# Kernel tuning notes

Hardware: AMD Instinct MI355X
Metric: run time of the kernel (lower is better)

## Reference

```python
import jax, jax.numpy as jnp
import numpy as np

N_NODES = 50000
N_EDGES = 400000
NUM_FEATURES = 128
NUM_CLASSES = 40
DIMS = [NUM_FEATURES, 1024, 512, 128]


def _glorot(key, shape):
    fan_in, fan_out = shape
    lim = jnp.sqrt(6.0 / (fan_in + fan_out))
    return jax.random.uniform(key, shape, jnp.float32, -lim, lim)


def setup_inputs() -> dict:
    key = jax.random.key(0)
    ks = jax.random.split(key, 12)
    x = jax.random.normal(ks[0], (N_NODES, NUM_FEATURES), jnp.float32)
    edge_index = jax.random.randint(ks[1], (2, N_EDGES), 0, N_NODES, jnp.int64)
    W1 = _glorot(ks[2], (DIMS[0], DIMS[1])); b1 = jnp.zeros((DIMS[1],), jnp.float32)
    W2 = _glorot(ks[3], (DIMS[1], DIMS[2])); b2 = jnp.zeros((DIMS[2],), jnp.float32)
    W3 = _glorot(ks[4], (DIMS[2], DIMS[3])); b3 = jnp.zeros((DIMS[3],), jnp.float32)
    Wfc = _glorot(ks[5], (DIMS[3], NUM_CLASSES))
    bfc = jnp.zeros((NUM_CLASSES,), jnp.float32)
    return {"x": x, "edge_index": edge_index, "W1": W1, "b1": b1,
            "W2": W2, "b2": b2, "W3": W3, "b3": b3, "Wfc": Wfc, "bfc": bfc}


def _gcn_conv(x, W, b, src, dst, norm, inv_deg, n_nodes):
    # GCNConv: transform, then symmetric-normalized aggregation with self-loops.
    h = x @ W                                   # [N, out]
    msg = h[src] * norm[:, None]                # [E, out] gathered + scaled
    agg = jax.ops.segment_sum(msg, dst, num_segments=n_nodes)
    agg = agg + h * inv_deg[:, None]            # self-loop term: d^-1 * h_i
    return agg + b


def reference(x, edge_index, W1, b1, W2, b2, W3, b3, Wfc, bfc):
    n = x.shape[0]
    src, dst = edge_index[0], edge_index[1]
    # degree including the self-loop (weight 1 per edge + 1 self-loop)
    deg = jax.ops.segment_sum(jnp.ones_like(dst, dtype=x.dtype), dst, num_segments=n) + 1.0
    inv_sqrt = jax.lax.rsqrt(deg)
    norm = inv_sqrt[src] * inv_sqrt[dst]        # [E]
    inv_deg = 1.0 / deg                         # self-loop norm d^-.5 * d^-.5

    h = jax.nn.relu(_gcn_conv(x, W1, b1, src, dst, norm, inv_deg, n))
    h = jax.nn.relu(_gcn_conv(h, W2, b2, src, dst, norm, inv_deg, n))
    h = jax.nn.relu(_gcn_conv(h, W3, b3, src, dst, norm, inv_deg, n))
    return h @ Wfc + bfc
```

## Files before the change

### kernel.cpp

```cpp
#include <hip/hip_runtime.h>
#include <hip/hip_bf16.h>
#include <cstdint>
#include <cstddef>

#define NN 50000
#define NE 400000
typedef long long i64;
typedef unsigned short u16;
typedef __attribute__((ext_vector_type(8))) short bf16x8;
typedef __attribute__((ext_vector_type(8))) unsigned short u16x8;
typedef __attribute__((ext_vector_type(4))) float f32x4;

__device__ inline u16 f2bf(float f) {
    unsigned u = __float_as_uint(f);
    u += 0x7fffu + ((u >> 16) & 1u);
    return (u16)(u >> 16);
}
__device__ inline float bf2f(u16 b) { return __uint_as_float(((unsigned)b) << 16); }

__global__ void k_init(int* __restrict__ deg, int* __restrict__ flag) {
    int i = blockIdx.x * blockDim.x + threadIdx.x;
    if (i < NN) deg[i] = 0;
    if (i == 0) *flag = 0;
}

__global__ void k_detect(const void* __restrict__ ei, int* __restrict__ flag) {
    int i = blockIdx.x * blockDim.x + threadIdx.x;
    if (i < NE) {
        i64 v = ((const i64*)ei)[i];
        if (v < 0 || v >= NN) atomicOr(flag, 1);
    }
}

__device__ inline int edge_at(const void* ei, int f32idx, int half, int i) {
    if (f32idx) return ((const int*)ei)[half * NE + i];
    return (int)((const i64*)ei)[half * NE + i];
}

__global__ void k_hist(const void* __restrict__ ei, const int* __restrict__ flag,
                       int* __restrict__ deg) {
    int i = blockIdx.x * blockDim.x + threadIdx.x;
    if (i < NE) {
        int d = edge_at(ei, *flag, 1, i);
        if ((unsigned)d < NN) atomicAdd(&deg[d], 1);
    }
}

__global__ void k_node_setup(const int* __restrict__ deg, float* __restrict__ inv_sqrt,
                             float* __restrict__ inv_deg) {
    int i = blockIdx.x * blockDim.x + threadIdx.x;
    if (i < NN) {
        float d = (float)deg[i] + 1.0f;
        inv_sqrt[i] = rsqrtf(d);
        inv_deg[i]  = 1.0f / d;
    }
}

#define SB 256
#define NBLK ((NN + SB - 1) / SB)

__global__ __launch_bounds__(SB) void k_scan1(const int* __restrict__ deg,
                                              int* __restrict__ excl,
                                              int* __restrict__ bsum) {
    __shared__ int s[SB];
    int t = threadIdx.x;
    int i = blockIdx.x * SB + t;
    int v = (i < NN) ? deg[i] : 0;
    s[t] = v;
    __syncthreads();
    for (int off = 1; off < SB; off <<= 1) {
        int x = (t >= off) ? s[t - off] : 0;
        __syncthreads();
        s[t] += x;
        __syncthreads();
    }
    if (i < NN) excl[i] = s[t] - v;
    if (t == SB - 1) bsum[blockIdx.x] = s[t];
}

__global__ __launch_bounds__(SB) void k_scan2(int* __restrict__ bsum) {
    __shared__ int s[SB];
    int t = threadIdx.x;
    int v = (t < NBLK) ? bsum[t] : 0;
    s[t] = v;
    __syncthreads();
    for (int off = 1; off < SB; off <<= 1) {
        int x = (t >= off) ? s[t - off] : 0;
        __syncthreads();
        s[t] += x;
        __syncthreads();
    }
    if (t < NBLK) bsum[t] = s[t] - v;
    if (t == NBLK - 1) bsum[NBLK] = s[t];
}

__global__ __launch_bounds__(SB) void k_scan3(int* __restrict__ row_off,
                                              int* __restrict__ cursor,
                                              const int* __restrict__ bsum) {
    int i = blockIdx.x * SB + threadIdx.x;
    if (i < NN) {
        int r = row_off[i] + bsum[blockIdx.x];
        row_off[i] = r;
        cursor[i]  = r;
    }
    if (i == 0) row_off[NN] = bsum[NBLK];
}

__global__ void k_scatter(const void* __restrict__ ei, const int* __restrict__ flag,
                          const float* __restrict__ inv_sqrt,
                          int* __restrict__ cursor, int* __restrict__ ssrc,
                          float* __restrict__ snorm) {
    int i = blockIdx.x * blockDim.x + threadIdx.x;
    if (i < NE) {
        int f = *flag;
        int s = edge_at(ei, f, 0, i);
        int d = edge_at(ei, f, 1, i);
        if ((unsigned)s < NN && (unsigned)d < NN) {
            int pos = atomicAdd(&cursor[d], 1);
            if ((unsigned)pos < NE) {
                ssrc[pos]  = s;
                snorm[pos] = inv_sqrt[s] * inv_sqrt[d];
            }
        }
    }
}

__global__ void k_wt(const float* __restrict__ W, u16* __restrict__ Wt, int K, int N) {
    int i = blockIdx.x * 256 + threadIdx.x;
    if (i < K * N) {
        int k = i / N, n = i - k * N;
        Wt[(size_t)n * K + k] = f2bf(W[i]);
    }
}

template <int W, int TIN, int TOUT, bool BIAS, bool RELU>
__global__ __launch_bounds__(64) void k_agg(const void* __restrict__ Xv, void* __restrict__ Yv,
                      const int* __restrict__ row_off, const int* __restrict__ ssrc,
                      const float* __restrict__ snorm, const float* __restrict__ inv_deg,
                      const float* __restrict__ bias) {
    constexpr int E = W / 64;
    int node = blockIdx.x;
    int lane = threadIdx.x;
    int col = lane * E;
    int beg = row_off[node], end = row_off[node + 1];
    float acc[E];
#pragma unroll
    for (int v = 0; v < E; v++) acc[v] = 0.f;

    auto accum = [&](int srow, float w) {
        if constexpr (TIN == 0) {
            const float* r = (const float*)Xv + (size_t)srow * W + col;
            if constexpr (E == 2) {
                float2 t = *(const float2*)r;
                acc[0] = fmaf(t.x, w, acc[0]);
                acc[1] = fmaf(t.y, w, acc[1]);
            } else {
                float4 t0 = *(const float4*)r;
                float4 t1 = *(const float4*)(r + 4);
                acc[0] = fmaf(t0.x, w, acc[0]); acc[1] = fmaf(t0.y, w, acc[1]);
                acc[2] = fmaf(t0.z, w, acc[2]); acc[3] = fmaf(t0.w, w, acc[3]);
                acc[4] = fmaf(t1.x, w, acc[4]); acc[5] = fmaf(t1.y, w, acc[5]);
                acc[6] = fmaf(t1.z, w, acc[6]); acc[7] = fmaf(t1.w, w, acc[7]);
            }
        } else {
            const u16* r = (const u16*)Xv + (size_t)srow * W + col;
            if constexpr (E == 2) {
                unsigned t = *(const unsigned*)r;
                acc[0] = fmaf(bf2f((u16)(t & 0xffff)), w, acc[0]);
                acc[1] = fmaf(bf2f((u16)(t >> 16)), w, acc[1]);
            } else {
                u16x8 t = *(const u16x8*)r;
#pragma unroll
                for (int j = 0; j < 8; j++) acc[j] = fmaf(bf2f(t[j]), w, acc[j]);
            }
        }
    };

    for (int e = beg; e < end; e++) {
        int s = ssrc[e];
        if ((unsigned)s >= NN) continue;
        accum(s, snorm[e]);
    }
    accum(node, inv_deg[node]);

#pragma unroll
    for (int v = 0; v < E; v++) {
        float val = acc[v];
        if (BIAS) val += bias[col + v];
        if (RELU) val = fmaxf(val, 0.f);
        if constexpr (TOUT == 0) ((float*)Yv)[(size_t)node * W + col + v] = val;
        else ((u16*)Yv)[(size_t)node * W + col + v] = f2bf(val);
    }
}

#define LDS_AS(p) ((__attribute__((address_space(3))) void*)(p))
#define GLB_AS(p) ((const __attribute__((address_space(1))) void*)(p))
#define EPAD 68

template <bool BIAS, bool RELU>
__global__ __launch_bounds__(512, 2) void gemm8(
    const u16* __restrict__ A, const u16* __restrict__ Bt,
    const float* __restrict__ bias, u16* __restrict__ C,
    int M, int N, int K, int nbx) {
    __shared__ __align__(16) char smem[131072];
    char* buf0 = smem;
    char* buf1 = smem + 65536;
    const int tid = threadIdx.x;
    const int lane = tid & 63;
    const int wave = tid >> 6;
    const int wm = wave >> 2;
    const int wn = wave & 3;

    const int nwg = gridDim.x;
    int lg;
    { int q = nwg >> 3, r = nwg & 7, xc = blockIdx.x & 7, pos = blockIdx.x >> 3;
      lg = (xc < r ? xc * (q + 1) : r * (q + 1) + (xc - r) * q) + pos; }
    const int bm = (lg / nbx) * 256;
    const int bn = (lg % nbx) * 256;

    f32x4 acc[8][4];
#pragma unroll
    for (int m = 0; m < 8; m++)
#pragma unroll
        for (int n = 0; n < 4; n++) acc[m][n] = (f32x4)0.f;

    const int rb = tid >> 3;
    const int csw = ((tid & 7) ^ (rb & 7)) << 4;
    const int dstA = rb * 128 + (tid & 7) * 16;
    const size_t sK = (size_t)K * 2;
    const char* Ab = (const char*)A;
    const char* Bb = (const char*)Bt;
    size_t ga[2][2], gb[2][2];
#pragma unroll
    for (int h = 0; h < 2; h++)
#pragma unroll
        for (int j = 0; j < 2; j++) {
            int ar = bm + h * 128 + j * 64 + rb; if (ar >= M) ar = M - 1;
            int br = bn + h * 128 + j * 64 + rb;
            ga[h][j] = (size_t)ar * sK + csw;
            gb[h][j] = (size_t)br * sK + csw;
        }

    auto stA = [&](char* buf, size_t kb, int h) {
        __builtin_amdgcn_global_load_lds(GLB_AS(Ab + ga[h][0] + kb), LDS_AS(buf + h * 16384 + dstA), 16, 0, 0);
        __builtin_amdgcn_global_load_lds(GLB_AS(Ab + ga[h][1] + kb), LDS_AS(buf + h * 16384 + 8192 + dstA), 16, 0, 0);
    };
    auto stB = [&](char* buf, size_t kb, int h) {
        __builtin_amdgcn_global_load_lds(GLB_AS(Bb + gb[h][0] + kb), LDS_AS(buf + 32768 + h * 16384 + dstA), 16, 0, 0);
        __builtin_amdgcn_global_load_lds(GLB_AS(Bb + gb[h][1] + kb), LDS_AS(buf + 32768 + h * 16384 + 8192 + dstA), 16, 0, 0);
    };

    const int fr = lane & 15, g = lane >> 4;
    const int ksw0 = (((0 << 2) + g) ^ (fr & 7)) << 4;
    const int ksw1 = (((1 << 2) + g) ^ (fr & 7)) << 4;
    const int aRow = (wm * 128 + fr) * 128;
    const int bRow = 32768 + (wn * 64 + fr) * 128;

    bf16x8 af[4][2], bf[4][2];
    auto LDA = [&](const char* buf, int mg) {
#pragma unroll
        for (int m = 0; m < 4; m++) {
            af[m][0] = *(const bf16x8*)(buf + aRow + mg * 8192 + m * 2048 + ksw0);
            af[m][1] = *(const bf16x8*)(buf + aRow + mg * 8192 + m * 2048 + ksw1);
        }
    };
    auto LDB = [&](const char* buf, int ng) {
#pragma unroll
        for (int n = 0; n < 2; n++) {
            bf[ng * 2 + n][0] = *(const bf16x8*)(buf + bRow + (ng * 2 + n) * 2048 + ksw0);
            bf[ng * 2 + n][1] = *(const bf16x8*)(buf + bRow + (ng * 2 + n) * 2048 + ksw1);
        }
    };
    auto QMM = [&](int mg, int ng) {
        __builtin_amdgcn_s_setprio(1);
#pragma unroll
        for (int ks = 0; ks < 2; ks++)
#pragma unroll
            for (int m = 0; m < 4; m++)
#pragma unroll
                for (int n = 0; n < 2; n++)
                    acc[mg * 4 + m][ng * 2 + n] = __builtin_amdgcn_mfma_f32_16x16x32_bf16(
                        af[m][ks], bf[ng * 2 + n][ks], acc[mg * 4 + m][ng * 2 + n], 0, 0, 0);
        __builtin_amdgcn_s_setprio(0);
    };

#define BAR  __builtin_amdgcn_s_barrier()
#define LGKM do { asm volatile("s_waitcnt lgkmcnt(0)" ::: "memory"); __builtin_amdgcn_sched_barrier(0); } while (0)

    const int nit = K >> 7;

    stB(buf0, 0, 0); stB(buf0, 0, 1);
    stA(buf0, 0, 0); stA(buf0, 0, 1);
    stB(buf1, 128, 0); stB(buf1, 128, 1);
    asm volatile("s_waitcnt vmcnt(4)" ::: "memory");
    BAR;

    for (int it2 = 0; it2 < nit; ++it2) {
        const bool lastit = (it2 == nit - 1);
        const size_t kb = (size_t)it2 * 256;
        LDA(buf0, 0); LDB(buf0, 0);
        stA(buf1, kb + 128, 0);
        BAR; LGKM; QMM(0, 0); BAR;
        LDB(buf0, 1);
        stA(buf1, kb + 128, 1);
        BAR; LGKM; QMM(0, 1); BAR;
        LDA(buf0, 1);
        if (!lastit) stB(buf0, kb + 256, 0);
        BAR; LGKM; QMM(1, 0); BAR;
        if (!lastit) stB(buf0, kb + 256, 1);
        BAR; QMM(1, 1);
        if (lastit) asm volatile("s_waitcnt vmcnt(0)" ::: "memory");
        else        asm volatile("s_waitcnt vmcnt(4)" ::: "memory");
        BAR;
        LDA(buf1, 0); LDB(buf1, 0);
        if (!lastit) stA(buf0, kb + 256, 0);
        BAR; LGKM; QMM(0, 0); BAR;
        LDB(buf1, 1);
        if (!lastit) stA(buf0, kb + 256, 1);
        BAR; LGKM; QMM(0, 1); BAR;
        LDA(buf1, 1);
        if (!lastit) stB(buf1, kb + 384, 0);
        BAR; LGKM; QMM(1, 0); BAR;
        if (!lastit) stB(buf1, kb + 384, 1);
        BAR; QMM(1, 1);
        if (!lastit) asm volatile("s_waitcnt vmcnt(4)" ::: "memory");
        BAR;
    }

    u16* Es = (u16*)(smem + (size_t)wave * (64 * EPAD * 2));
    const int cr = (lane >> 4) << 2;
    const int cc = lane & 15;
    const int rl = lane >> 3;
    const int c8 = (lane & 7) * 8;
#pragma unroll
    for (int pass = 0; pass < 2; pass++) {
#pragma unroll
        for (int n = 0; n < 4; n++) {
            float bv = BIAS ? bias[bn + wn * 64 + n * 16 + cc] : 0.f;
#pragma unroll
            for (int m = 0; m < 4; m++) {
#pragma unroll
                for (int j = 0; j < 4; j++) {
                    float v = acc[pass * 4 + m][n][j] + bv;
                    if (RELU) v = fmaxf(v, 0.f);
                    Es[(m * 16 + cr + j) * EPAD + n * 16 + cc] = f2bf(v);
                }
            }
        }
#pragma unroll
        for (int itr = 0; itr < 8; itr++) {
            int lr = itr * 8 + rl;
            u16x8 vv = *(const u16x8*)(Es + lr * EPAD + c8);
            int grow = bm + wm * 128 + pass * 64 + lr;
            if (grow < M)
                *(u16x8*)(C + (size_t)grow * N + bn + wn * 64 + c8) = vv;
        }
    }
#undef BAR
#undef LGKM
}

#define GBM 128
#define GBN 128
#define GBK 64

template <bool BIAS, bool RELU>
__global__ __launch_bounds__(256) void mfma_gemm(
    const u16* __restrict__ A, const u16* __restrict__ Bt,
    const float* __restrict__ bias, u16* __restrict__ C,
    int M, int N, int K, int nbx) {
    __shared__ __align__(16) char smem[4 * 64 * EPAD * 2];
    u16* As = (u16*)smem;
    u16* Bs = (u16*)(smem + 16384);
    const int tid = threadIdx.x;
    const int lane = tid & 63;
    const int wave = tid >> 6;
    const int wr = wave >> 1, wc = wave & 1;

    const int nwg = gridDim.x;
    int lg;
    { int q = nwg >> 3, r = nwg & 7, xc = blockIdx.x & 7, pos = blockIdx.x >> 3;
      lg = (xc < r ? xc * (q + 1) : r * (q + 1) + (xc - r) * q) + pos; }
    const int bm = (lg / nbx) * GBM;
    const int bn = (lg % nbx) * GBN;

    f32x4 acc[4][4];
#pragma unroll
    for (int m = 0; m < 4; m++)
#pragma unroll
        for (int n = 0; n < 4; n++) acc[m][n] = (f32x4)0.f;

    const int rbase = tid >> 3;
    const int csw = (((tid & 7) ^ (rbase & 7)) << 4);
    const size_t sK = (size_t)K * 2;
    const char* Ab = (const char*)A;
    const char* Bb = (const char*)Bt;
    size_t ga[4], gb[4];
#pragma unroll
    for (int i = 0; i < 4; i++) {
        int r0 = rbase + 32 * i;
        int ar = bm + r0; if (ar >= M) ar = M - 1;
        int br = bn + r0; if (br >= N) br = N - 1;
        ga[i] = (size_t)ar * sK + csw;
        gb[i] = (size_t)br * sK + csw;
    }
    const int od = tid * 16;

    const int fr = lane & 15, g = lane >> 4;
    int aoff[2][4], boff[2][4];
#pragma unroll
    for (int ks = 0; ks < 2; ks++) {
        const int sw = (((ks << 2) + g) ^ (fr & 7)) << 4;
#pragma unroll
        for (int m = 0; m < 4; m++) {
            aoff[ks][m] = (wr * 64 + m * 16 + fr) * 128 + sw;
            boff[ks][m] = (wc * 64 + m * 16 + fr) * 128 + sw;
        }
    }

    for (int k0 = 0; k0 < K; k0 += GBK) {
        const size_t kb = (size_t)k0 * 2;
#pragma unroll
        for (int i = 0; i < 4; i++) {
            __builtin_amdgcn_global_load_lds(GLB_AS(Ab + ga[i] + kb), LDS_AS((char*)As + od + i * 4096), 16, 0, 0);
            __builtin_amdgcn_global_load_lds(GLB_AS(Bb + gb[i] + kb), LDS_AS((char*)Bs + od + i * 4096), 16, 0, 0);
        }
        __syncthreads();
#pragma unroll
        for (int ks = 0; ks < 2; ks++) {
            bf16x8 af[4], bfr[4];
#pragma unroll
            for (int n = 0; n < 4; n++) bfr[n] = *(const bf16x8*)((char*)Bs + boff[ks][n]);
#pragma unroll
            for (int m = 0; m < 4; m++) af[m] = *(const bf16x8*)((char*)As + aoff[ks][m]);
#pragma unroll
            for (int m = 0; m < 4; m++)
#pragma unroll
                for (int n = 0; n < 4; n++)
                    acc[m][n] = __builtin_amdgcn_mfma_f32_16x16x32_bf16(af[m], bfr[n], acc[m][n], 0, 0, 0);
        }
        __syncthreads();
    }

    u16* Es = (u16*)smem + (size_t)wave * 64 * EPAD;
    const int cr = (lane >> 4) << 2;
    const int cc = lane & 15;
#pragma unroll
    for (int n = 0; n < 4; n++) {
        float bv = BIAS ? bias[bn + wc * 64 + n * 16 + cc] : 0.f;
#pragma unroll
        for (int m = 0; m < 4; m++) {
#pragma unroll
            for (int j = 0; j < 4; j++) {
                float v = acc[m][n][j] + bv;
                if (RELU) v = fmaxf(v, 0.f);
                Es[(m * 16 + cr + j) * EPAD + n * 16 + cc] = f2bf(v);
            }
        }
    }
    const int rl = lane >> 3;
    const int c8 = (lane & 7) * 8;
#pragma unroll
    for (int it = 0; it < 8; it++) {
        int lr = it * 8 + rl;
        u16x8 vv = *(const u16x8*)(Es + lr * EPAD + c8);
        int grow = bm + wr * 64 + lr;
        if (grow < M)
            *(u16x8*)(C + (size_t)grow * N + bn + wc * 64 + c8) = vv;
    }
}

#define TBM 64
#define TBN 64
#define TBK 16
#define LPAD 4

template <bool BIAS, bool RELU>
__global__ __launch_bounds__(256) void gemm_kernel(
    const float* __restrict__ A, const float* __restrict__ B,
    const float* __restrict__ bias, float* __restrict__ C,
    int M, int N, int K) {
    __shared__ float Asl[TBK][TBM + LPAD];
    __shared__ float Bsl[TBK][TBN + LPAD];
    const int bm = blockIdx.y * TBM;
    const int bn = blockIdx.x * TBN;
    const int tid = threadIdx.x;
    const int tx = tid & 15;
    const int ty = tid >> 4;
    const int la_m = tid >> 2;
    const int la_k = (tid & 3) << 2;
    const int lb_k = tid >> 4;
    const int lb_n = (tid & 15) << 2;

    float acc[4][4];
#pragma unroll
    for (int i = 0; i < 4; i++)
#pragma unroll
        for (int j = 0; j < 4; j++) acc[i][j] = 0.f;

    const int am = bm + la_m;
    const bool a_ok = am < M;
    const int bng = bn + lb_n;

    for (int k0 = 0; k0 < K; k0 += TBK) {
        float4 av = make_float4(0.f, 0.f, 0.f, 0.f);
        if (a_ok) av = *(const float4*)(A + (size_t)am * K + k0 + la_k);
        float4 bv = make_float4(0.f, 0.f, 0.f, 0.f);
        {
            const float* Bp = B + (size_t)(k0 + lb_k) * N + bng;
            if (bng + 3 < N) {
                bv = *(const float4*)Bp;
            } else {
                if (bng + 0 < N) bv.x = Bp[0];
                if (bng + 1 < N) bv.y = Bp[1];
                if (bng + 2 < N) bv.z = Bp[2];
            }
        }
        Asl[la_k + 0][la_m] = av.x;
        Asl[la_k + 1][la_m] = av.y;
        Asl[la_k + 2][la_m] = av.z;
        Asl[la_k + 3][la_m] = av.w;
        *(float4*)&Bsl[lb_k][lb_n] = bv;
        __syncthreads();
#pragma unroll
        for (int k = 0; k < TBK; k++) {
            float4 a = *(const float4*)&Asl[k][ty << 2];
            float4 b = *(const float4*)&Bsl[k][tx << 2];
            float aa[4] = {a.x, a.y, a.z, a.w};
            float bb[4] = {b.x, b.y, b.z, b.w};
#pragma unroll
            for (int i = 0; i < 4; i++)
#pragma unroll
                for (int j = 0; j < 4; j++)
                    acc[i][j] = fmaf(aa[i], bb[j], acc[i][j]);
        }
        __syncthreads();
    }
#pragma unroll
    for (int i = 0; i < 4; i++) {
        int m = bm + (ty << 2) + i;
        if (m < M) {
#pragma unroll
            for (int j = 0; j < 4; j++) {
                int n = bn + (tx << 2) + j;
                if (n < N) {
                    float v = acc[i][j];
                    if (BIAS) v += bias[n];
                    if (RELU) v = fmaxf(v, 0.f);
                    C[(size_t)m * N + n] = v;
                }
            }
        }
    }
}

extern "C" void kernel_launch(void* const* d_in, const int* in_sizes, int n_in,
                              void* d_out, int out_size, void* d_ws, size_t ws_size,
                              hipStream_t stream) {
    const float* x   = (const float*)d_in[0];
    const void*  ei  = d_in[1];
    const float* W1  = (const float*)d_in[2];
    const float* b1  = (const float*)d_in[3];
    const float* W2  = (const float*)d_in[4];
    const float* b2  = (const float*)d_in[5];
    const float* W3  = (const float*)d_in[6];
    const float* b3  = (const float*)d_in[7];
    const float* Wfc = (const float*)d_in[8];
    const float* bfc = (const float*)d_in[9];
    float* out = (float*)d_out;

    char* ws = (char*)d_ws;
    size_t off = 0;
    auto take = [&](size_t bytes) -> void* {
        off = (off + 255) & ~(size_t)255;
        void* p = ws + off;
        off += bytes;
        return p;
    };
    int*   deg     = (int*)take((size_t)NN * 4);
    int*   row_off = (int*)take((size_t)(NN + 1) * 4);
    int*   cursor  = (int*)take((size_t)NN * 4);
    float* isq     = (float*)take((size_t)NN * 4);
    float* idg     = (float*)take((size_t)NN * 4);
    int*   ssrc    = (int*)take((size_t)NE * 4);
    float* snorm   = (float*)take((size_t)NE * 4);
    int*   flag    = (int*)take(256);
    int*   bsum    = (int*)take((size_t)(NBLK + 1) * 4);
    u16*   Wt1     = (u16*)take((size_t)1024 * 128 * 2);
    u16*   Wt2     = (u16*)take((size_t)512 * 1024 * 2);
    u16*   Wt3     = (u16*)take((size_t)128 * 512 * 2);
    u16*   rA      = (u16*)take((size_t)NN * 128 * 2);
    u16*   rH      = (u16*)take((size_t)NN * 1024 * 2);
    u16*   rT      = (u16*)take((size_t)NN * 512 * 2);
    float* h3      = (float*)take((size_t)NN * 128 * 4);

    k_init<<<(NN + 255) / 256, 256, 0, stream>>>(deg, flag);
    k_detect<<<(NE + 255) / 256, 256, 0, stream>>>(ei, flag);
    k_hist<<<(NE + 255) / 256, 256, 0, stream>>>(ei, flag, deg);
    k_node_setup<<<(NN + 255) / 256, 256, 0, stream>>>(deg, isq, idg);
    k_scan1<<<NBLK, SB, 0, stream>>>(deg, row_off, bsum);
    k_scan2<<<1, SB, 0, stream>>>(bsum);
    k_scan3<<<NBLK, SB, 0, stream>>>(row_off, cursor, bsum);
    k_scatter<<<(NE + 255) / 256, 256, 0, stream>>>(ei, flag, isq, cursor, ssrc, snorm);

    k_wt<<<(128 * 1024 + 255) / 256, 256, 0, stream>>>(W1, Wt1, 128, 1024);
    k_wt<<<(1024 * 512 + 255) / 256, 256, 0, stream>>>(W2, Wt2, 1024, 512);
    k_wt<<<(512 * 128 + 255) / 256, 256, 0, stream>>>(W3, Wt3, 512, 128);

    const int MB256 = (NN + 255) / 256;
    const int MB128 = (NN + 127) / 128;

    u16* a0 = rA;
    k_agg<128, 0, 1, false, false><<<NN, 64, 0, stream>>>(x, a0, row_off, ssrc, snorm, idg, nullptr);
    u16* h1 = rH;
    gemm8<true, true><<<MB256 * 4, 512, 0, stream>>>(a0, Wt1, b1, h1, NN, 1024, 128, 4);

    u16* t2 = rT;
    gemm8<false, false><<<MB256 * 2, 512, 0, stream>>>(h1, Wt2, nullptr, t2, NN, 512, 1024, 2);
    u16* h2 = rH;
    k_agg<512, 1, 1, true, true><<<NN, 64, 0, stream>>>(t2, h2, row_off, ssrc, snorm, idg, b2);

    u16* g3 = rA;
    mfma_gemm<false, false><<<MB128, 256, 0, stream>>>(h2, Wt3, nullptr, g3, NN, 128, 512, 1);
    k_agg<128, 1, 0, true, true><<<NN, 64, 0, stream>>>(g3, h3, row_off, ssrc, snorm, idg, b3);

    gemm_kernel<true, false><<<dim3(1, (NN + TBM - 1) / TBM), 256, 0, stream>>>(h3, Wfc, bfc, out, NN, 40, 128);

    (void)in_sizes; (void)n_in; (void)out_size; (void)ws_size;
}
```

Before: 432.3 us.

## Replace layer-1 and layer-3 GEMMs with LDS-free direct-load MFMA kernel

Adds a gemm_direct kernel in which each wave loads its A and B MFMA fragments straight from global memory into registers, with no LDS staging and no barriers. It uses 64-row tiles and WN waves per block. It replaces gemm8 for the K=128 first-layer GEMM and mfma_gemm for the K=512 third-layer GEMM, aiming to cut barrier and LDS overhead on these short-K products and to raise occupancy with smaller blocks. In exchange it gives up data reuse across waves, since every wave re-reads the same A rows from global memory or cache, and the fragment loads are uncoalesced strided 16-byte reads.

```diff
diff --git a/kernel.cpp b/kernel.cpp
--- a/kernel.cpp
+++ b/kernel.cpp
@@ -196,6 +196,88 @@
 #define LDS_AS(p) ((__attribute__((address_space(3))) void*)(p))
 #define GLB_AS(p) ((const __attribute__((address_space(1))) void*)(p))
 #define EPAD 68
+
+template <int WN, bool BIAS, bool RELU>
+__global__ __launch_bounds__(WN * 64, 4) void gemm_direct(
+    const u16* __restrict__ A, const u16* __restrict__ Bt,
+    const float* __restrict__ bias, u16* __restrict__ C,
+    int M, int N, int K, int nbx) {
+    __shared__ __align__(16) char smem[WN * 64 * EPAD * 2];
+    const int tid = threadIdx.x;
+    const int lane = tid & 63;
+    const int wn = tid >> 6;
+
+    const int nwg = gridDim.x;
+    int lg;
+    { int q = nwg >> 3, r = nwg & 7, xc = blockIdx.x & 7, pos = blockIdx.x >> 3;
+      lg = (xc < r ? xc * (q + 1) : r * (q + 1) + (xc - r) * q) + pos; }
+    const int bm = (lg / nbx) * 64;
+    const int bn = (lg % nbx) * (WN * 64);
+
+    const int fr = lane & 15, g = lane >> 4;
+    const size_t sK = (size_t)K * 2;
+    const char* Ab = (const char*)A;
+    const char* Bb = (const char*)Bt;
+    const char* ap[4];
+    const char* bp[4];
+#pragma unroll
+    for (int m = 0; m < 4; m++) {
+        int ar = bm + m * 16 + fr; if (ar >= M) ar = M - 1;
+        ap[m] = Ab + (size_t)ar * sK + g * 16;
+        int br = bn + wn * 64 + m * 16 + fr;
+        bp[m] = Bb + (size_t)br * sK + g * 16;
+    }
+
+    f32x4 acc[4][4];
+#pragma unroll
+    for (int m = 0; m < 4; m++)
+#pragma unroll
+        for (int n = 0; n < 4; n++) acc[m][n] = (f32x4)0.f;
+
+    for (int kc = 0; kc < K; kc += 128) {
+#pragma unroll
+        for (int ks = 0; ks < 4; ks++) {
+            const int ko = kc * 2 + ks * 64;
+            bf16x8 af[4], bf[4];
+#pragma unroll
+            for (int m = 0; m < 4; m++) af[m] = *(const bf16x8*)(ap[m] + ko);
+#pragma unroll
+            for (int n = 0; n < 4; n++) bf[n] = *(const bf16x8*)(bp[n] + ko);
+#pragma unroll
+            for (int m = 0; m < 4; m++)
+#pragma unroll
+                for (int n = 0; n < 4; n++)
+                    acc[m][n] = __builtin_amdgcn_mfma_f32_16x16x32_bf16(af[m], bf[n], acc[m][n], 0, 0, 0);
+        }
+    }
+
+    u16* Es = (u16*)(smem + (size_t)wn * (64 * EPAD * 2));
+    const int cr = (lane >> 4) << 2;
+    const int cc = lane & 15;
+#pragma unroll
+    for (int n = 0; n < 4; n++) {
+        float bv = BIAS ? bias[bn + wn * 64 + n * 16 + cc] : 0.f;
+#pragma unroll
+        for (int m = 0; m < 4; m++) {
+#pragma unroll
+            for (int j = 0; j < 4; j++) {
+                float v = acc[m][n][j] + bv;
+                if (RELU) v = fmaxf(v, 0.f);
+                Es[(m * 16 + cr + j) * EPAD + n * 16 + cc] = f2bf(v);
+            }
+        }
+    }
+    const int rl = lane >> 3;
+    const int c8 = (lane & 7) * 8;
+#pragma unroll
+    for (int it = 0; it < 8; it++) {
+        int lr = it * 8 + rl;
+        u16x8 vv = *(const u16x8*)(Es + lr * EPAD + c8);
+        int grow = bm + lr;
+        if (grow < M)
+            *(u16x8*)(C + (size_t)grow * N + bn + wn * 64 + c8) = vv;
+    }
+}
 
 template <bool BIAS, bool RELU>
 __global__ __launch_bounds__(512, 2) void gemm8(
@@ -360,116 +442,6 @@
 #undef LGKM
 }
 
-#define GBM 128
-#define GBN 128
-#define GBK 64
-
-template <bool BIAS, bool RELU>
-__global__ __launch_bounds__(256) void mfma_gemm(
-    const u16* __restrict__ A, const u16* __restrict__ Bt,
-    const float* __restrict__ bias, u16* __restrict__ C,
-    int M, int N, int K, int nbx) {
-    __shared__ __align__(16) char smem[4 * 64 * EPAD * 2];
-    u16* As = (u16*)smem;
-    u16* Bs = (u16*)(smem + 16384);
-    const int tid = threadIdx.x;
-    const int lane = tid & 63;
-    const int wave = tid >> 6;
-    const int wr = wave >> 1, wc = wave & 1;
-
-    const int nwg = gridDim.x;
-    int lg;
-    { int q = nwg >> 3, r = nwg & 7, xc = blockIdx.x & 7, pos = blockIdx.x >> 3;
-      lg = (xc < r ? xc * (q + 1) : r * (q + 1) + (xc - r) * q) + pos; }
-    const int bm = (lg / nbx) * GBM;
-    const int bn = (lg % nbx) * GBN;
-
-    f32x4 acc[4][4];
-#pragma unroll
-    for (int m = 0; m < 4; m++)
-#pragma unroll
-        for (int n = 0; n < 4; n++) acc[m][n] = (f32x4)0.f;
-
-    const int rbase = tid >> 3;
-    const int csw = (((tid & 7) ^ (rbase & 7)) << 4);
-    const size_t sK = (size_t)K * 2;
-    const char* Ab = (const char*)A;
-    const char* Bb = (const char*)Bt;
-    size_t ga[4], gb[4];
-#pragma unroll
-    for (int i = 0; i < 4; i++) {
-        int r0 = rbase + 32 * i;
-        int ar = bm + r0; if (ar >= M) ar = M - 1;
-        int br = bn + r0; if (br >= N) br = N - 1;
-        ga[i] = (size_t)ar * sK + csw;
-        gb[i] = (size_t)br * sK + csw;
-    }
-    const int od = tid * 16;
-
-    const int fr = lane & 15, g = lane >> 4;
-    int aoff[2][4], boff[2][4];
-#pragma unroll
-    for (int ks = 0; ks < 2; ks++) {
-        const int sw = (((ks << 2) + g) ^ (fr & 7)) << 4;
-#pragma unroll
-        for (int m = 0; m < 4; m++) {
-            aoff[ks][m] = (wr * 64 + m * 16 + fr) * 128 + sw;
-            boff[ks][m] = (wc * 64 + m * 16 + fr) * 128 + sw;
-        }
-    }
-
-    for (int k0 = 0; k0 < K; k0 += GBK) {
-        const size_t kb = (size_t)k0 * 2;
-#pragma unroll
-        for (int i = 0; i < 4; i++) {
-            __builtin_amdgcn_global_load_lds(GLB_AS(Ab + ga[i] + kb), LDS_AS((char*)As + od + i * 4096), 16, 0, 0);
-            __builtin_amdgcn_global_load_lds(GLB_AS(Bb + gb[i] + kb), LDS_AS((char*)Bs + od + i * 4096), 16, 0, 0);
-        }
-        __syncthreads();
-#pragma unroll
-        for (int ks = 0; ks < 2; ks++) {
-            bf16x8 af[4], bfr[4];
-#pragma unroll
-            for (int n = 0; n < 4; n++) bfr[n] = *(const bf16x8*)((char*)Bs + boff[ks][n]);
-#pragma unroll
-            for (int m = 0; m < 4; m++) af[m] = *(const bf16x8*)((char*)As + aoff[ks][m]);
-#pragma unroll
-            for (int m = 0; m < 4; m++)
-#pragma unroll
-                for (int n = 0; n < 4; n++)
-                    acc[m][n] = __builtin_amdgcn_mfma_f32_16x16x32_bf16(af[m], bfr[n], acc[m][n], 0, 0, 0);
-        }
-        __syncthreads();
-    }
-
-    u16* Es = (u16*)smem + (size_t)wave * 64 * EPAD;
-    const int cr = (lane >> 4) << 2;
-    const int cc = lane & 15;
-#pragma unroll
-    for (int n = 0; n < 4; n++) {
-        float bv = BIAS ? bias[bn + wc * 64 + n * 16 + cc] : 0.f;
-#pragma unroll
-        for (int m = 0; m < 4; m++) {
-#pragma unroll
-            for (int j = 0; j < 4; j++) {
-                float v = acc[m][n][j] + bv;
-                if (RELU) v = fmaxf(v, 0.f);
-                Es[(m * 16 + cr + j) * EPAD + n * 16 + cc] = f2bf(v);
-            }
-        }
-    }
-    const int rl = lane >> 3;
-    const int c8 = (lane & 7) * 8;
-#pragma unroll
-    for (int it = 0; it < 8; it++) {
-        int lr = it * 8 + rl;
-        u16x8 vv = *(const u16x8*)(Es + lr * EPAD + c8);
-        int grow = bm + wr * 64 + lr;
-        if (grow < M)
-            *(u16x8*)(C + (size_t)grow * N + bn + wc * 64 + c8) = vv;
-    }
-}
-
 #define TBM 64
 #define TBN 64
 #define TBK 16
@@ -608,12 +580,12 @@
     k_wt<<<(512 * 128 + 255) / 256, 256, 0, stream>>>(W3, Wt3, 512, 128);
 
     const int MB256 = (NN + 255) / 256;
-    const int MB128 = (NN + 127) / 128;
+    const int MB64  = (NN + 63) / 64;
 
     u16* a0 = rA;
     k_agg<128, 0, 1, false, false><<<NN, 64, 0, stream>>>(x, a0, row_off, ssrc, snorm, idg, nullptr);
     u16* h1 = rH;
-    gemm8<true, true><<<MB256 * 4, 512, 0, stream>>>(a0, Wt1, b1, h1, NN, 1024, 128, 4);
+    gemm_direct<4, true, true><<<MB64 * 4, 256, 0, stream>>>(a0, Wt1, b1, h1, NN, 1024, 128, 4);
 
     u16* t2 = rT;
     gemm8<false, false><<<MB256 * 2, 512, 0, stream>>>(h1, Wt2, nullptr, t2, NN, 512, 1024, 2);
@@ -621,7 +593,7 @@
     k_agg<512, 1, 1, true, true><<<NN, 64, 0, stream>>>(t2, h2, row_off, ssrc, snorm, idg, b2);
 
     u16* g3 = rA;
-    mfma_gemm<false, false><<<MB128, 256, 0, stream>>>(h2, Wt3, nullptr, g3, NN, 128, 512, 1);
+    gemm_direct<2, false, false><<<MB64, 128, 0, stream>>>(h2, Wt3, nullptr, g3, NN, 128, 512, 1);
     k_agg<128, 1, 0, true, true><<<NN, 64, 0, stream>>>(g3, h3, row_off, ssrc, snorm, idg, b3);
 
     gemm_kernel<true, false><<<dim3(1, (NN + TBM - 1) / TBM), 256, 0, stream>>>(h3, Wfc, bfc, out, NN, 40, 128);
```

Result: slower. 464.9 us (+7.5%).

## Fuse final aggregation with FC layer and gather layer-1 input in bf16

Applied to the files above, without the earlier changes.

The third-layer aggregation now computes bias+ReLU into shared memory and immediately applies the 128x40 FC projection per node, so the fp32 h3 buffer is never written or reread and the separate FC GEMM is gone. The input features are also converted to bf16 once up front, so the first aggregation gathers half as many bytes per edge. This adds a conversion pass over x, and the fused FC runs as 40 lanes each doing a 128-step dot product per node with Wfc read from global/L2, which may be slow per block.

```diff
diff --git a/kernel.cpp b/kernel.cpp
--- a/kernel.cpp
+++ b/kernel.cpp
@@ -9,6 +9,7 @@
 typedef unsigned short u16;
 typedef __attribute__((ext_vector_type(8))) short bf16x8;
 typedef __attribute__((ext_vector_type(8))) unsigned short u16x8;
+typedef __attribute__((ext_vector_type(4))) unsigned short u16x4;
 typedef __attribute__((ext_vector_type(4))) float f32x4;
 
 __device__ inline u16 f2bf(float f) {
@@ -130,6 +131,16 @@
     if (i < K * N) {
         int k = i / N, n = i - k * N;
         Wt[(size_t)n * K + k] = f2bf(W[i]);
+    }
+}
+
+__global__ void k_x2bf(const float* __restrict__ x, u16* __restrict__ xb, int n4) {
+    int i = blockIdx.x * 256 + threadIdx.x;
+    if (i < n4) {
+        float4 v = ((const float4*)x)[i];
+        u16x4 r;
+        r[0] = f2bf(v.x); r[1] = f2bf(v.y); r[2] = f2bf(v.z); r[3] = f2bf(v.w);
+        ((u16x4*)xb)[i] = r;
     }
 }
 
@@ -190,6 +201,44 @@
         if (RELU) val = fmaxf(val, 0.f);
         if constexpr (TOUT == 0) ((float*)Yv)[(size_t)node * W + col + v] = val;
         else ((u16*)Yv)[(size_t)node * W + col + v] = f2bf(val);
+    }
+}
+
+__global__ __launch_bounds__(64) void k_agg_fc(const u16* __restrict__ X,
+                      float* __restrict__ out,
+                      const int* __restrict__ row_off, const int* __restrict__ ssrc,
+                      const float* __restrict__ snorm, const float* __restrict__ inv_deg,
+                      const float* __restrict__ b3, const float* __restrict__ Wfc,
+                      const float* __restrict__ bfc) {
+    __shared__ float hrow[128];
+    int node = blockIdx.x;
+    int lane = threadIdx.x;
+    int col = lane * 2;
+    int beg = row_off[node], end = row_off[node + 1];
+    float a0 = 0.f, a1 = 0.f;
+    for (int e = beg; e < end; e++) {
+        int s = ssrc[e];
+        if ((unsigned)s >= NN) continue;
+        float w = snorm[e];
+        unsigned t = *(const unsigned*)(X + (size_t)s * 128 + col);
+        a0 = fmaf(bf2f((u16)(t & 0xffff)), w, a0);
+        a1 = fmaf(bf2f((u16)(t >> 16)), w, a1);
+    }
+    {
+        float w = inv_deg[node];
+        unsigned t = *(const unsigned*)(X + (size_t)node * 128 + col);
+        a0 = fmaf(bf2f((u16)(t & 0xffff)), w, a0);
+        a1 = fmaf(bf2f((u16)(t >> 16)), w, a1);
+    }
+    hrow[col]     = fmaxf(a0 + b3[col], 0.f);
+    hrow[col + 1] = fmaxf(a1 + b3[col + 1], 0.f);
+    __syncthreads();
+    if (lane < 40) {
+        float s = bfc[lane];
+#pragma unroll 8
+        for (int k = 0; k < 128; k++)
+            s = fmaf(hrow[k], Wfc[k * 40 + lane], s);
+        out[(size_t)node * 40 + lane] = s;
     }
 }
 
@@ -470,90 +519,6 @@
     }
 }
 
-#define TBM 64
-#define TBN 64
-#define TBK 16
-#define LPAD 4
-
-template <bool BIAS, bool RELU>
-__global__ __launch_bounds__(256) void gemm_kernel(
-    const float* __restrict__ A, const float* __restrict__ B,
-    const float* __restrict__ bias, float* __restrict__ C,
-    int M, int N, int K) {
-    __shared__ float Asl[TBK][TBM + LPAD];
-    __shared__ float Bsl[TBK][TBN + LPAD];
-    const int bm = blockIdx.y * TBM;
-    const int bn = blockIdx.x * TBN;
-    const int tid = threadIdx.x;
-    const int tx = tid & 15;
-    const int ty = tid >> 4;
-    const int la_m = tid >> 2;
-    const int la_k = (tid & 3) << 2;
-    const int lb_k = tid >> 4;
-    const int lb_n = (tid & 15) << 2;
-
-    float acc[4][4];
-#pragma unroll
-    for (int i = 0; i < 4; i++)
-#pragma unroll
-        for (int j = 0; j < 4; j++) acc[i][j] = 0.f;
-
-    const int am = bm + la_m;
-    const bool a_ok = am < M;
-    const int bng = bn + lb_n;
-
-    for (int k0 = 0; k0 < K; k0 += TBK) {
-        float4 av = make_float4(0.f, 0.f, 0.f, 0.f);
-        if (a_ok) av = *(const float4*)(A + (size_t)am * K + k0 + la_k);
-        float4 bv = make_float4(0.f, 0.f, 0.f, 0.f);
-        {
-            const float* Bp = B + (size_t)(k0 + lb_k) * N + bng;
-            if (bng + 3 < N) {
-                bv = *(const float4*)Bp;
-            } else {
-                if (bng + 0 < N) bv.x = Bp[0];
-                if (bng + 1 < N) bv.y = Bp[1];
-                if (bng + 2 < N) bv.z = Bp[2];
-            }
-        }
-        Asl[la_k + 0][la_m] = av.x;
-        Asl[la_k + 1][la_m] = av.y;
-        Asl[la_k + 2][la_m] = av.z;
-        Asl[la_k + 3][la_m] = av.w;
-        *(float4*)&Bsl[lb_k][lb_n] = bv;
-        __syncthreads();
-#pragma unroll
-        for (int k = 0; k < TBK; k++) {
-            float4 a = *(const float4*)&Asl[k][ty << 2];
-            float4 b = *(const float4*)&Bsl[k][tx << 2];
-            float aa[4] = {a.x, a.y, a.z, a.w};
-            float bb[4] = {b.x, b.y, b.z, b.w};
-#pragma unroll
-            for (int i = 0; i < 4; i++)
-#pragma unroll
-                for (int j = 0; j < 4; j++)
-                    acc[i][j] = fmaf(aa[i], bb[j], acc[i][j]);
-        }
-        __syncthreads();
-    }
-#pragma unroll
-    for (int i = 0; i < 4; i++) {
-        int m = bm + (ty << 2) + i;
-        if (m < M) {
-#pragma unroll
-            for (int j = 0; j < 4; j++) {
-                int n = bn + (tx << 2) + j;
-                if (n < N) {
-                    float v = acc[i][j];
-                    if (BIAS) v += bias[n];
-                    if (RELU) v = fmaxf(v, 0.f);
-                    C[(size_t)m * N + n] = v;
-                }
-            }
-        }
-    }
-}
-
 extern "C" void kernel_launch(void* const* d_in, const int* in_sizes, int n_in,
                               void* d_out, int out_size, void* d_ws, size_t ws_size,
                               hipStream_t stream) {
@@ -589,10 +554,10 @@
     u16*   Wt1     = (u16*)take((size_t)1024 * 128 * 2);
     u16*   Wt2     = (u16*)take((size_t)512 * 1024 * 2);
     u16*   Wt3     = (u16*)take((size_t)128 * 512 * 2);
+    u16*   xbf     = (u16*)take((size_t)NN * 128 * 2);
     u16*   rA      = (u16*)take((size_t)NN * 128 * 2);
     u16*   rH      = (u16*)take((size_t)NN * 1024 * 2);
     u16*   rT      = (u16*)take((size_t)NN * 512 * 2);
-    float* h3      = (float*)take((size_t)NN * 128 * 4);
 
     k_init<<<(NN + 255) / 256, 256, 0, stream>>>(deg, flag);
     k_detect<<<(NE + 255) / 256, 256, 0, stream>>>(ei, flag);
@@ -606,12 +571,13 @@
     k_wt<<<(128 * 1024 + 255) / 256, 256, 0, stream>>>(W1, Wt1, 128, 1024);
     k_wt<<<(1024 * 512 + 255) / 256, 256, 0, stream>>>(W2, Wt2, 1024, 512);
     k_wt<<<(512 * 128 + 255) / 256, 256, 0, stream>>>(W3, Wt3, 512, 128);
+    k_x2bf<<<(NN * 128 / 4 + 255) / 256, 256, 0, stream>>>(x, xbf, NN * 128 / 4);
 
     const int MB256 = (NN + 255) / 256;
     const int MB128 = (NN + 127) / 128;
 
     u16* a0 = rA;
-    k_agg<128, 0, 1, false, false><<<NN, 64, 0, stream>>>(x, a0, row_off, ssrc, snorm, idg, nullptr);
+    k_agg<128, 1, 1, false, false><<<NN, 64, 0, stream>>>(xbf, a0, row_off, ssrc, snorm, idg, nullptr);
     u16* h1 = rH;
     gemm8<true, true><<<MB256 * 4, 512, 0, stream>>>(a0, Wt1, b1, h1, NN, 1024, 128, 4);
 
@@ -622,9 +588,7 @@
 
     u16* g3 = rA;
     mfma_gemm<false, false><<<MB128, 256, 0, stream>>>(h2, Wt3, nullptr, g3, NN, 128, 512, 1);
-    k_agg<128, 1, 0, true, true><<<NN, 64, 0, stream>>>(g3, h3, row_off, ssrc, snorm, idg, b3);
-
-    gemm_kernel<true, false><<<dim3(1, (NN + TBM - 1) / TBM), 256, 0, stream>>>(h3, Wfc, bfc, out, NN, 40, 128);
+    k_agg_fc<<<NN, 64, 0, stream>>>(g3, out, row_off, ssrc, snorm, idg, b3, Wfc, bfc);
 
     (void)in_sizes; (void)n_in; (void)out_size; (void)ws_size;
 }
```

Result: slower. 445.6 us (+3.1%).
